# Performance work log

Hardware: AMD Instinct MI355X
Metric: run time of the kernel (lower is better)

## Reference

```python
import jax, jax.numpy as jnp
import numpy as np

H, DH = 16, 64  # heads, dim_head

def _ln(x, g, b):
    mu = jnp.mean(x, axis=-1, keepdims=True)
    var = jnp.var(x, axis=-1, keepdims=True)
    return (x - mu) * jax.lax.rsqrt(var + 1e-5) * g + b

def setup_inputs() -> dict:
    key = jax.random.key(0)
    ks = jax.random.split(key, 6)
    B, N1, N2, D = 8, 4096, 256, 1024
    inner = H * DH
    x = jax.random.normal(ks[0], (B, N1, D), jnp.float32)
    latents = jax.random.normal(ks[1], (B, N2, D), jnp.float32)
    mask = jnp.ones((B, N1 + N2), jnp.int32)
    Wq = jax.random.normal(ks[2], (D, inner), jnp.float32) / np.float32(np.sqrt(D))
    Wkv = jax.random.normal(ks[3], (D, 2 * inner), jnp.float32) / np.float32(np.sqrt(D))
    Wout = jax.random.normal(ks[4], (inner, D), jnp.float32) / np.float32(np.sqrt(inner))
    g_media = jnp.ones((D,), jnp.float32)
    b_media = jnp.zeros((D,), jnp.float32)
    g_lat = jnp.ones((D,), jnp.float32)
    b_lat = jnp.zeros((D,), jnp.float32)
    return {"x": x, "latents": latents, "mask": mask,
            "g_media": g_media, "b_media": b_media, "g_lat": g_lat, "b_lat": b_lat,
            "Wq": Wq, "Wkv": Wkv, "Wout": Wout}

def reference(x, latents, mask, g_media, b_media, g_lat, b_lat, Wq, Wkv, Wout):
    scale = DH ** -0.5
    xn = _ln(x, g_media, b_media)            # (B, N1, D)
    ln = _ln(latents, g_lat, b_lat)          # (B, N2, D)
    q = ln @ Wq                              # (B, N2, H*DH)
    kv = jnp.concatenate([xn, ln], axis=1) @ Wkv  # (B, N1+N2, 2*H*DH)
    k, v = jnp.split(kv, 2, axis=-1)
    B, N2 = q.shape[0], q.shape[1]
    Nk = k.shape[1]
    q = q.reshape(B, N2, H, DH).transpose(0, 2, 1, 3) * scale  # (B,H,N2,DH)
    k = k.reshape(B, Nk, H, DH).transpose(0, 2, 1, 3)
    v = v.reshape(B, Nk, H, DH).transpose(0, 2, 1, 3)
    sim = jnp.einsum('bhid,bhjd->bhij', q, k)                  # (B,H,N2,Nk)
    sim = sim - jax.lax.stop_gradient(jnp.max(sim, axis=-1, keepdims=True))
    sim = jnp.where(mask[:, None, None, :] == 0, jnp.float32(-10000.0), sim)
    attn = jax.nn.softmax(sim, axis=-1)
    out = jnp.einsum('bhij,bhjd->bhid', attn, v)               # (B,H,N2,DH)
    out = out.transpose(0, 2, 1, 3).reshape(B, N2, H * DH)
    return out @ Wout                                          # (B, N2, D)
```

## Files before the change

kernel.cpp:

```cpp
#include <hip/hip_runtime.h>
#include <stdint.h>

typedef __attribute__((ext_vector_type(4))) float f32x4;
typedef __attribute__((ext_vector_type(4))) int   i32x4;

__device__ __forceinline__ ushort f2bf(float f) {
  union { float f; uint32_t u; } v; v.f = f;
  uint32_t r = v.u + 0x7FFFu + ((v.u >> 16) & 1u);
  return (ushort)(r >> 16);
}
__device__ __forceinline__ float bf2f(ushort u) {
  union { uint32_t u; float f; } v; v.u = ((uint32_t)u) << 16; return v.f;
}
__device__ __forceinline__ void mfma_acc(f32x4& c, i32x4 a, i32x4 b) {
  asm volatile("v_mfma_f32_16x16x32_bf16 %0, %1, %2, %0" : "+v"(c) : "v"(a), "v"(b));
}
__device__ __forceinline__ void gload_lds16(const void* g, void* lds) {
  __builtin_amdgcn_global_load_lds(
      (const __attribute__((address_space(1))) void*)g,
      (__attribute__((address_space(3))) void*)lds, 16, 0, 0);
}

__global__ void __launch_bounds__(256) ln_kernel(
    const float* __restrict__ x, const float* __restrict__ lat,
    const float* __restrict__ gm, const float* __restrict__ bm,
    const float* __restrict__ gl, const float* __restrict__ bl,
    ushort* __restrict__ out) {
  int row = blockIdx.x;
  int b = row / 4352, j = row - b * 4352;
  const float *src, *g, *bi;
  if (j < 4096) { src = x + ((size_t)b * 4096 + j) * 1024; g = gm; bi = bm; }
  else          { src = lat + ((size_t)b * 256 + (j - 4096)) * 1024; g = gl; bi = bl; }
  int t = threadIdx.x;
  f32x4 v = ((const f32x4*)src)[t];
  float s = v.x + v.y + v.z + v.w;
  float q = v.x * v.x + v.y * v.y + v.z * v.z + v.w * v.w;
  #pragma unroll
  for (int o = 1; o < 64; o <<= 1) { s += __shfl_xor(s, o, 64); q += __shfl_xor(q, o, 64); }
  __shared__ float ss[4], sq[4];
  int w = t >> 6, l = t & 63;
  if (l == 0) { ss[w] = s; sq[w] = q; }
  __syncthreads();
  s = ss[0] + ss[1] + ss[2] + ss[3];
  q = sq[0] + sq[1] + sq[2] + sq[3];
  float mu = s * (1.f / 1024.f);
  float var = q * (1.f / 1024.f) - mu * mu;
  float rs = rsqrtf(var + 1e-5f);
  f32x4 gg = ((const f32x4*)g)[t], bb = ((const f32x4*)bi)[t];
  ushort4 o4;
  o4.x = f2bf((v.x - mu) * rs * gg.x + bb.x);
  o4.y = f2bf((v.y - mu) * rs * gg.y + bb.y);
  o4.z = f2bf((v.z - mu) * rs * gg.z + bb.z);
  o4.w = f2bf((v.w - mu) * rs * gg.w + bb.w);
  ((ushort4*)(out + (size_t)row * 1024))[t] = o4;
}

__global__ void __launch_bounds__(256) tsplit_kernel(
    const float* __restrict__ W, int K, int N, ushort* __restrict__ out, int K2, int write_lo) {
  int ntn = N >> 6;
  int tk = blockIdx.x / ntn, tn = blockIdx.x - tk * ntn;
  int k0 = tk * 32, n0 = tn * 64;
  __shared__ float tile[32][65];
  int t = threadIdx.x;
  #pragma unroll
  for (int i = 0; i < 8; i++) {
    int idx = t + i * 256;
    int k = idx >> 6, n = idx & 63;
    tile[k][n] = W[(size_t)(k0 + k) * N + n0 + n];
  }
  __syncthreads();
  #pragma unroll
  for (int i = 0; i < 8; i++) {
    int idx = t + i * 256;
    int n = idx >> 5, k = idx & 31;
    float v = tile[k][n];
    ushort hi = f2bf(v);
    size_t o = (size_t)(n0 + n) * K2 + k0 + k;
    out[o] = hi;
    if (write_lo) out[o + K] = f2bf(v - bf2f(hi));
  }
}

__global__ void __launch_bounds__(512, 2) gemm256_kv(
    const ushort* __restrict__ A, const ushort* __restrict__ Bw,
    ushort* __restrict__ okb, ushort* __restrict__ ovb) {
  int orig = blockIdx.x;
  int bx = (orig & 7) * 136 + (orig >> 3);
  int mt = bx >> 3, nt = bx & 7;
  int m0 = mt * 256, n0 = nt * 256;
  int t = threadIdx.x, w = t >> 6, l = t & 63, lg = l >> 4, lr = l & 15;
  int wr = w >> 2, wc = w & 3;

  __shared__ char smem[131072];

  auto stage = [&](int kt, int bsel) {
    size_t ka = (size_t)kt * 64;
    char* sA = smem + bsel * 65536;
    char* sB = smem + bsel * 65536 + 32768;
    #pragma unroll
    for (int i = 0; i < 4; i++) {
      int c = t + i * 512;
      int row = c >> 3, j = c & 7;
      int sj = j ^ (row & 7);
      gload_lds16(A + ((size_t)(m0 + row) * 1024 + ka + sj * 8), sA + c * 16);
    }
    #pragma unroll
    for (int i = 0; i < 4; i++) {
      int c = t + i * 512;
      int row = c >> 3, j = c & 7;
      int sj = j ^ (row & 7);
      gload_lds16(Bw + ((size_t)(n0 + row) * 1024 + ka + sj * 8), sB + c * 16);
    }
  };

  f32x4 acc[8][4];
  #pragma unroll
  for (int i = 0; i < 8; i++)
    #pragma unroll
    for (int j = 0; j < 4; j++) acc[i][j] = (f32x4){0.f, 0.f, 0.f, 0.f};

  stage(0, 0);
  stage(1, 1);
  const int swz = (lr & 7) << 4;

  for (int kt = 0; kt < 16; kt++) {
    if (kt < 15) asm volatile("s_waitcnt vmcnt(8)" ::: "memory");
    else         asm volatile("s_waitcnt vmcnt(0)" ::: "memory");
    __builtin_amdgcn_s_barrier();
    const char* cA = smem + (kt & 1) * 65536;
    const char* cB = smem + (kt & 1) * 65536 + 32768;
    i32x4 ar[4][2], br[4][2];
    #pragma unroll
    for (int mi = 0; mi < 4; mi++)
      #pragma unroll
      for (int kk = 0; kk < 2; kk++)
        ar[mi][kk] = *(const i32x4*)(cA + ((((wr * 128 + mi * 16 + lr) * 128) + kk * 64 + lg * 16) ^ swz));
    #pragma unroll
    for (int nj = 0; nj < 2; nj++)
      #pragma unroll
      for (int kk = 0; kk < 2; kk++)
        br[nj][kk] = *(const i32x4*)(cB + ((((wc * 64 + nj * 16 + lr) * 128) + kk * 64 + lg * 16) ^ swz));
    __builtin_amdgcn_s_setprio(1);
    #pragma unroll
    for (int mi = 0; mi < 4; mi++)
      #pragma unroll
      for (int nj = 0; nj < 2; nj++)
        #pragma unroll
        for (int kk = 0; kk < 2; kk++) mfma_acc(acc[mi][nj], ar[mi][kk], br[nj][kk]);
    __builtin_amdgcn_s_setprio(0);
    #pragma unroll
    for (int nj = 2; nj < 4; nj++)
      #pragma unroll
      for (int kk = 0; kk < 2; kk++)
        br[nj][kk] = *(const i32x4*)(cB + ((((wc * 64 + nj * 16 + lr) * 128) + kk * 64 + lg * 16) ^ swz));
    __builtin_amdgcn_s_setprio(1);
    #pragma unroll
    for (int mi = 0; mi < 4; mi++)
      #pragma unroll
      for (int nj = 2; nj < 4; nj++)
        #pragma unroll
        for (int kk = 0; kk < 2; kk++) mfma_acc(acc[mi][nj], ar[mi][kk], br[nj][kk]);
    __builtin_amdgcn_s_setprio(0);
    #pragma unroll
    for (int mi = 0; mi < 4; mi++)
      #pragma unroll
      for (int kk = 0; kk < 2; kk++)
        ar[mi][kk] = *(const i32x4*)(cA + ((((wr * 128 + (mi + 4) * 16 + lr) * 128) + kk * 64 + lg * 16) ^ swz));
    __builtin_amdgcn_s_setprio(1);
    #pragma unroll
    for (int mi = 0; mi < 4; mi++)
      #pragma unroll
      for (int nj = 2; nj < 4; nj++)
        #pragma unroll
        for (int kk = 0; kk < 2; kk++) mfma_acc(acc[mi + 4][nj], ar[mi][kk], br[nj][kk]);
    __builtin_amdgcn_s_setprio(0);
    __builtin_amdgcn_s_setprio(1);
    #pragma unroll
    for (int mi = 0; mi < 4; mi++)
      #pragma unroll
      for (int nj = 0; nj < 2; nj++)
        #pragma unroll
        for (int kk = 0; kk < 2; kk++) mfma_acc(acc[mi + 4][nj], ar[mi][kk], br[nj][kk]);
    __builtin_amdgcn_s_setprio(0);
    __builtin_amdgcn_s_barrier();
    if (kt + 2 < 16) stage(kt + 2, kt & 1);
  }

  #pragma unroll
  for (int mi = 0; mi < 8; mi++) {
    #pragma unroll
    for (int r = 0; r < 4; r++) {
      int row = m0 + wr * 128 + mi * 16 + lg * 4 + r;
      int b = row / 4352; int n = row - b * 4352;
      size_t base = (size_t)b * 4456448 + (size_t)n * 64;
      #pragma unroll
      for (int nj = 0; nj < 4; nj++) {
        int col = n0 + wc * 64 + nj * 16 + lr;
        int cc = col & 1023; int h = cc >> 6; int d = cc & 63;
        ushort* dst = (col < 1024) ? okb : ovb;
        dst[base + (size_t)h * 278528 + d] = f2bf(acc[mi][nj][r]);
      }
    }
  }
}

template<int MODE>
__global__ void __launch_bounds__(256, 2) gemm_nt(
    const ushort* __restrict__ A, const ushort* __restrict__ Bw,
    ushort* __restrict__ okb, float* __restrict__ of,
    int ntn, int Keff, int lda, int ldb) {
  int orig = blockIdx.x;
  int bx = ((orig & 7) * (gridDim.x >> 3)) + (orig >> 3);
  int m0 = (bx / ntn) * 128, n0 = (bx - (bx / ntn) * ntn) * 128;
  int t = threadIdx.x, w = t >> 6, l = t & 63, lg = l >> 4, lr = l & 15;
  int wr = w >> 1, wc = w & 1;
  __shared__ ushort As[128 * 32];
  __shared__ ushort Bs[128 * 32];
  f32x4 acc[4][4];
  #pragma unroll
  for (int i = 0; i < 4; i++)
    #pragma unroll
    for (int j = 0; j < 4; j++) acc[i][j] = (f32x4){0.f, 0.f, 0.f, 0.f};

  int nk = Keff >> 5;
  for (int kt = 0; kt < nk; kt++) {
    int ka = kt * 32;
    #pragma unroll
    for (int c2 = 0; c2 < 2; c2++) {
      int c = w * 2 + c2;
      int arow = m0 + c * 16 + (l >> 2);
      if (MODE == 1) arow = ((arow >> 8) * 4352) + 4096 + (arow & 255);
      gload_lds16(A + (size_t)arow * lda + ka + (l & 3) * 8, &As[c * 512]);
    }
    #pragma unroll
    for (int c2 = 0; c2 < 2; c2++) {
      int c = w * 2 + c2;
      int brow = n0 + c * 16 + (l >> 2);
      gload_lds16(Bw + (size_t)brow * ldb + ka + (l & 3) * 8, &Bs[c * 512]);
    }
    __syncthreads();
    i32x4 af[4], bf[4];
    #pragma unroll
    for (int mi = 0; mi < 4; mi++)
      af[mi] = *(const i32x4*)&As[(wr * 64 + mi * 16 + lr) * 32 + lg * 8];
    #pragma unroll
    for (int nj = 0; nj < 4; nj++)
      bf[nj] = *(const i32x4*)&Bs[(wc * 64 + nj * 16 + lr) * 32 + lg * 8];
    #pragma unroll
    for (int mi = 0; mi < 4; mi++)
      #pragma unroll
      for (int nj = 0; nj < 4; nj++) mfma_acc(acc[mi][nj], af[mi], bf[nj]);
    __syncthreads();
  }

  #pragma unroll
  for (int mi = 0; mi < 4; mi++) {
    #pragma unroll
    for (int r = 0; r < 4; r++) {
      int row = m0 + wr * 64 + mi * 16 + lg * 4 + r;
      if (MODE == 1) {
        int b = row >> 8; int n2 = row & 255;
        size_t base = (size_t)b * 262144 + (size_t)n2 * 64;
        #pragma unroll
        for (int nj = 0; nj < 4; nj++) {
          int col = n0 + wc * 64 + nj * 16 + lr;
          int h = col >> 6; int d = col & 63;
          okb[base + (size_t)h * 16384 + d] = f2bf(acc[mi][nj][r] * 0.125f);
        }
      } else {
        #pragma unroll
        for (int nj = 0; nj < 4; nj++) {
          int col = n0 + wc * 64 + nj * 16 + lr;
          of[(size_t)row * 1024 + col] = acc[mi][nj][r];
        }
      }
    }
  }
}

__global__ void __launch_bounds__(256) vtrans_kernel(const ushort* __restrict__ v,
                                                     ushort* __restrict__ vt) {
  int bh = blockIdx.x / 68, tk = blockIdx.x - bh * 68;
  __shared__ ushort tl[64][65];
  int t = threadIdx.x;
  const ushort* src = v + (size_t)bh * 278528 + (size_t)tk * 4096;
  #pragma unroll
  for (int c2 = 0; c2 < 2; c2++) {
    int idx = t + c2 * 256;
    int row = idx >> 3, cb = idx & 7;
    i32x4 d4 = *(const i32x4*)(src + row * 64 + cb * 8);
    const ushort* p = (const ushort*)&d4;
    #pragma unroll
    for (int e = 0; e < 8; e++) tl[row][cb * 8 + e] = p[e];
  }
  __syncthreads();
  ushort* dst = vt + (size_t)bh * 278528 + tk * 64;
  #pragma unroll
  for (int i = 0; i < 16; i++) {
    int idx = t + i * 256;
    int d = idx >> 6, key = idx & 63;
    dst[(size_t)d * 4352 + key] = tl[key][d];
  }
}

__global__ void __launch_bounds__(256, 2) attn_kernel(
    const ushort* __restrict__ qb, const ushort* __restrict__ kb,
    const ushort* __restrict__ vt, const int* __restrict__ mask,
    ushort* __restrict__ ao) {
  int orig = blockIdx.x;
  int bid = ((orig & 7) << 6) + (orig >> 3);
  int qt = bid & 3; int h = (bid >> 2) & 15; int b = bid >> 6;
  int t = threadIdx.x, w = t >> 6, l = t & 63, lg = l >> 4, lr = l & 15;
  __shared__ ushort Kl[2][4096];
  __shared__ ushort Vl[2][4096];
  __shared__ ushort Pl[64 * 72];
  __shared__ float bias[4352];
  size_t bh = (size_t)b * 16 + h;
  const ushort* qhead = qb + bh * 16384 + (size_t)qt * 4096;
  const ushort* khead = kb + bh * 278528;
  const ushort* vthead = vt + bh * 278528;

  #pragma unroll
  for (int c2 = 0; c2 < 2; c2++) {
    int c = w * 2 + c2;
    int row = c * 8 + (l >> 3);
    int colb = ((l & 7) * 16) ^ ((row & 7) << 4);
    gload_lds16((const char*)qhead + row * 128 + colb, (char*)Kl + c * 1024);
  }
  for (int i = t; i < 4352; i += 256)
    bias[i] = mask[b * 4352 + i] ? -24.0f : -10024.0f;
  __syncthreads();
  i32x4 aq[2];
  #pragma unroll
  for (int kh = 0; kh < 2; kh++) {
    int row = w * 16 + lr;
    int off = (row * 128 + kh * 64 + lg * 16) ^ ((row & 7) << 4);
    aq[kh] = *(const i32x4*)((const char*)Kl + off);
  }
  __syncthreads();

  auto stage = [&](int tk, int bsel) {
    #pragma unroll
    for (int c2 = 0; c2 < 2; c2++) {
      int c = w * 2 + c2;
      int row = c * 8 + (l >> 3);
      int colb = ((l & 7) * 16) ^ ((row & 7) << 4);
      gload_lds16((const char*)khead + (size_t)(tk * 64 + row) * 128 + colb,
                  (char*)Kl + bsel * 8192 + c * 1024);
      gload_lds16((const char*)vthead + (size_t)row * 8704 + (size_t)tk * 128 + colb,
                  (char*)Vl + bsel * 8192 + c * 1024);
    }
  };

  float lsum[4];
  f32x4 oacc[4];
  #pragma unroll
  for (int r = 0; r < 4; r++) lsum[r] = 0.f;
  #pragma unroll
  for (int df = 0; df < 4; df++) oacc[df] = (f32x4){0.f, 0.f, 0.f, 0.f};

  stage(0, 0);
  int cur = 0;
  for (int tk = 0; tk < 68; tk++) {
    if (tk < 67) {
      stage(tk + 1, cur ^ 1);
      asm volatile("s_waitcnt vmcnt(4)" ::: "memory");
    } else {
      asm volatile("s_waitcnt vmcnt(0)" ::: "memory");
    }
    asm volatile("s_barrier" ::: "memory");
    const char* Kb = (const char*)Kl + cur * 8192;
    const char* Vb = (const char*)Vl + cur * 8192;

    f32x4 sf[4];
    #pragma unroll
    for (int kf = 0; kf < 4; kf++) {
      f32x4 s = (f32x4){0.f, 0.f, 0.f, 0.f};
      #pragma unroll
      for (int kh = 0; kh < 2; kh++) {
        int row = kf * 16 + lr;
        int off = (row * 128 + kh * 64 + lg * 16) ^ ((row & 7) << 4);
        i32x4 bk = *(const i32x4*)(Kb + off);
        mfma_acc(s, aq[kh], bk);
      }
      sf[kf] = s;
    }
    #pragma unroll
    for (int kf = 0; kf < 4; kf++) {
      float ma = bias[tk * 64 + kf * 16 + lr];
      #pragma unroll
      for (int r = 0; r < 4; r++) {
        float p = __expf(sf[kf][r] + ma);
        lsum[r] += p;
        Pl[(w * 16 + lg * 4 + r) * 72 + kf * 16 + lr] = f2bf(p);
      }
    }
    #pragma unroll
    for (int kq = 0; kq < 2; kq++) {
      i32x4 ap = *(const i32x4*)&Pl[(w * 16 + lr) * 72 + kq * 32 + lg * 8];
      #pragma unroll
      for (int df = 0; df < 4; df++) {
        int row = df * 16 + lr;
        int off = (row * 128 + kq * 64 + lg * 16) ^ ((row & 7) << 4);
        i32x4 bv = *(const i32x4*)(Vb + off);
        mfma_acc(oacc[df], ap, bv);
      }
    }
    asm volatile("s_barrier" ::: "memory");
    cur ^= 1;
  }
  #pragma unroll
  for (int o = 1; o < 16; o <<= 1)
    #pragma unroll
    for (int r = 0; r < 4; r++) lsum[r] += __shfl_xor(lsum[r], o, 64);
  #pragma unroll
  for (int r = 0; r < 4; r++) lsum[r] = 1.f / lsum[r];
  int n2 = qt * 64 + w * 16 + lg * 4;
  #pragma unroll
  for (int df = 0; df < 4; df++)
    #pragma unroll
    for (int r = 0; r < 4; r++) {
      float vv = oacc[df][r] * lsum[r];
      ao[((size_t)b * 256 + (n2 + r)) * 1024 + h * 64 + df * 16 + lr] = f2bf(vv);
    }
}

extern "C" void kernel_launch(void* const* d_in, const int* in_sizes, int n_in,
                              void* d_out, int out_size, void* d_ws, size_t ws_size,
                              hipStream_t stream) {
  const float* x    = (const float*)d_in[0];
  const float* lat  = (const float*)d_in[1];
  const int*   msk  = (const int*)d_in[2];
  const float* gm   = (const float*)d_in[3];
  const float* bm   = (const float*)d_in[4];
  const float* gl   = (const float*)d_in[5];
  const float* bl   = (const float*)d_in[6];
  const float* Wq   = (const float*)d_in[7];
  const float* Wkv  = (const float*)d_in[8];
  const float* Wout = (const float*)d_in[9];
  float* out = (float*)d_out;
  char* ws = (char*)d_ws;

  ushort* xcat  = (ushort*)(ws);
  ushort* kbuf  = (ushort*)(ws + 71303168);
  ushort* vbuf  = (ushort*)(ws + 142606336);
  ushort* qbuf  = (ushort*)(ws + 213909504);
  ushort* aobuf = (ushort*)(ws + 218103808);
  ushort* wkvt  = (ushort*)(ws + 222298112);
  ushort* wqt   = (ushort*)(ws + 226492416);
  ushort* wot   = (ushort*)(ws + 228589568);
  ushort* vt    = xcat;

  ln_kernel<<<34816, 256, 0, stream>>>(x, lat, gm, bm, gl, bl, xcat);
  tsplit_kernel<<<32 * 32, 256, 0, stream>>>(Wkv, 1024, 2048, wkvt, 1024, 0);
  tsplit_kernel<<<32 * 16, 256, 0, stream>>>(Wq, 1024, 1024, wqt, 1024, 0);
  tsplit_kernel<<<32 * 16, 256, 0, stream>>>(Wout, 1024, 1024, wot, 1024, 0);
  gemm256_kv<<<1088, 512, 0, stream>>>(xcat, wkvt, kbuf, vbuf);
  gemm_nt<1><<<16 * 8, 256, 0, stream>>>(xcat, wqt, qbuf, nullptr, 8, 1024, 1024, 1024);
  vtrans_kernel<<<128 * 68, 256, 0, stream>>>(vbuf, vt);
  attn_kernel<<<512, 256, 0, stream>>>(qbuf, kbuf, vt, msk, aobuf);
  gemm_nt<2><<<16 * 8, 256, 0, stream>>>(aobuf, wot, nullptr, out, 8, 1024, 1024, 1024);
}
```

Before: 378.1 us.

## Fuse V transpose into KV GEMM epilogue via LDS staging

The KV GEMM epilogue now writes V directly in transposed (d-major) layout by staging each wave's accumulator tile in shared memory and emitting 16-byte vector stores, which removes the separate vtrans kernel and its extra global read/write of V. The inner MFMA loop is also reordered so all B fragments load up front and A rows 4-7 load into separate registers, changing register pressure and LDS read scheduling. Rows that cross a batch boundary fall back to scalar stores.

```diff
diff --git a/kernel.cpp b/kernel.cpp
--- a/kernel.cpp
+++ b/kernel.cpp
@@ -129,50 +129,42 @@
     __builtin_amdgcn_s_barrier();
     const char* cA = smem + (kt & 1) * 65536;
     const char* cB = smem + (kt & 1) * 65536 + 32768;
-    i32x4 ar[4][2], br[4][2];
+    i32x4 a03[4][2], a47[4][2], b01[2][2], b23[2][2];
     #pragma unroll
     for (int mi = 0; mi < 4; mi++)
       #pragma unroll
       for (int kk = 0; kk < 2; kk++)
-        ar[mi][kk] = *(const i32x4*)(cA + ((((wr * 128 + mi * 16 + lr) * 128) + kk * 64 + lg * 16) ^ swz));
+        a03[mi][kk] = *(const i32x4*)(cA + ((((wr * 128 + mi * 16 + lr) * 128) + kk * 64 + lg * 16) ^ swz));
     #pragma unroll
     for (int nj = 0; nj < 2; nj++)
       #pragma unroll
       for (int kk = 0; kk < 2; kk++)
-        br[nj][kk] = *(const i32x4*)(cB + ((((wc * 64 + nj * 16 + lr) * 128) + kk * 64 + lg * 16) ^ swz));
+        b01[nj][kk] = *(const i32x4*)(cB + ((((wc * 64 + nj * 16 + lr) * 128) + kk * 64 + lg * 16) ^ swz));
+    #pragma unroll
+    for (int nj = 0; nj < 2; nj++)
+      #pragma unroll
+      for (int kk = 0; kk < 2; kk++)
+        b23[nj][kk] = *(const i32x4*)(cB + ((((wc * 64 + (nj + 2) * 16 + lr) * 128) + kk * 64 + lg * 16) ^ swz));
     __builtin_amdgcn_s_setprio(1);
     #pragma unroll
     for (int mi = 0; mi < 4; mi++)
       #pragma unroll
       for (int nj = 0; nj < 2; nj++)
         #pragma unroll
-        for (int kk = 0; kk < 2; kk++) mfma_acc(acc[mi][nj], ar[mi][kk], br[nj][kk]);
+        for (int kk = 0; kk < 2; kk++) mfma_acc(acc[mi][nj], a03[mi][kk], b01[nj][kk]);
     __builtin_amdgcn_s_setprio(0);
     #pragma unroll
-    for (int nj = 2; nj < 4; nj++)
+    for (int mi = 0; mi < 4; mi++)
       #pragma unroll
       for (int kk = 0; kk < 2; kk++)
-        br[nj][kk] = *(const i32x4*)(cB + ((((wc * 64 + nj * 16 + lr) * 128) + kk * 64 + lg * 16) ^ swz));
+        a47[mi][kk] = *(const i32x4*)(cA + ((((wr * 128 + (mi + 4) * 16 + lr) * 128) + kk * 64 + lg * 16) ^ swz));
     __builtin_amdgcn_s_setprio(1);
     #pragma unroll
     for (int mi = 0; mi < 4; mi++)
       #pragma unroll
-      for (int nj = 2; nj < 4; nj++)
-        #pragma unroll
-        for (int kk = 0; kk < 2; kk++) mfma_acc(acc[mi][nj], ar[mi][kk], br[nj][kk]);
-    __builtin_amdgcn_s_setprio(0);
-    #pragma unroll
-    for (int mi = 0; mi < 4; mi++)
-      #pragma unroll
-      for (int kk = 0; kk < 2; kk++)
-        ar[mi][kk] = *(const i32x4*)(cA + ((((wr * 128 + (mi + 4) * 16 + lr) * 128) + kk * 64 + lg * 16) ^ swz));
-    __builtin_amdgcn_s_setprio(1);
-    #pragma unroll
-    for (int mi = 0; mi < 4; mi++)
-      #pragma unroll
-      for (int nj = 2; nj < 4; nj++)
-        #pragma unroll
-        for (int kk = 0; kk < 2; kk++) mfma_acc(acc[mi + 4][nj], ar[mi][kk], br[nj][kk]);
+      for (int nj = 0; nj < 2; nj++)
+        #pragma unroll
+        for (int kk = 0; kk < 2; kk++) mfma_acc(acc[mi][nj + 2], a03[mi][kk], b23[nj][kk]);
     __builtin_amdgcn_s_setprio(0);
     __builtin_amdgcn_s_setprio(1);
     #pragma unroll
@@ -180,25 +172,71 @@
       #pragma unroll
       for (int nj = 0; nj < 2; nj++)
         #pragma unroll
-        for (int kk = 0; kk < 2; kk++) mfma_acc(acc[mi + 4][nj], ar[mi][kk], br[nj][kk]);
+        for (int kk = 0; kk < 2; kk++) mfma_acc(acc[mi + 4][nj + 2], a47[mi][kk], b23[nj][kk]);
+    __builtin_amdgcn_s_setprio(0);
+    __builtin_amdgcn_s_setprio(1);
+    #pragma unroll
+    for (int mi = 0; mi < 4; mi++)
+      #pragma unroll
+      for (int nj = 0; nj < 2; nj++)
+        #pragma unroll
+        for (int kk = 0; kk < 2; kk++) mfma_acc(acc[mi + 4][nj], a47[mi][kk], b01[nj][kk]);
     __builtin_amdgcn_s_setprio(0);
     __builtin_amdgcn_s_barrier();
     if (kt + 2 < 16) stage(kt + 2, kt & 1);
   }
 
-  #pragma unroll
-  for (int mi = 0; mi < 8; mi++) {
-    #pragma unroll
-    for (int r = 0; r < 4; r++) {
-      int row = m0 + wr * 128 + mi * 16 + lg * 4 + r;
-      int b = row / 4352; int n = row - b * 4352;
-      size_t base = (size_t)b * 4456448 + (size_t)n * 64;
-      #pragma unroll
-      for (int nj = 0; nj < 4; nj++) {
-        int col = n0 + wc * 64 + nj * 16 + lr;
-        int cc = col & 1023; int h = cc >> 6; int d = cc & 63;
-        ushort* dst = (col < 1024) ? okb : ovb;
-        dst[base + (size_t)h * 278528 + d] = f2bf(acc[mi][nj][r]);
+  if (n0 < 1024) {
+    #pragma unroll
+    for (int mi = 0; mi < 8; mi++) {
+      #pragma unroll
+      for (int r = 0; r < 4; r++) {
+        int row = m0 + wr * 128 + mi * 16 + lg * 4 + r;
+        int b = row / 4352; int n = row - b * 4352;
+        size_t base = (size_t)b * 4456448 + (size_t)n * 64;
+        #pragma unroll
+        for (int nj = 0; nj < 4; nj++) {
+          int col = n0 + wc * 64 + nj * 16 + lr;
+          int h = col >> 6; int d = col & 63;
+          okb[base + (size_t)h * 278528 + d] = f2bf(acc[mi][nj][r]);
+        }
+      }
+    }
+  } else {
+    ushort* trp = (ushort*)(smem + w * 8704);
+    int hh = ((n0 - 1024) + wc * 64) >> 6;
+    size_t hoff = (size_t)hh * 278528;
+    #pragma unroll
+    for (int p = 0; p < 2; p++) {
+      #pragma unroll
+      for (int njd = 0; njd < 2; njd++)
+        #pragma unroll
+        for (int mi = 0; mi < 8; mi++)
+          #pragma unroll
+          for (int r = 0; r < 4; r++)
+            trp[(njd * 16 + lr) * 136 + mi * 16 + lg * 4 + r] = f2bf(acc[mi][p * 2 + njd][r]);
+      #pragma unroll
+      for (int it = 0; it < 8; it++) {
+        int c = it * 4 + (l >> 4);
+        int rr8 = (l & 15) * 8;
+        i32x4 vdat = *(const i32x4*)&trp[c * 136 + rr8];
+        int d = p * 32 + c;
+        int row_g = m0 + wr * 128 + rr8;
+        int b0 = row_g / 4352;
+        int b7 = (row_g + 7) / 4352;
+        if (b0 == b7) {
+          size_t n = row_g - b0 * 4352;
+          *(i32x4*)(ovb + (size_t)b0 * 4456448 + hoff + (size_t)d * 4352 + n) = vdat;
+        } else {
+          const ushort* pv = (const ushort*)&vdat;
+          #pragma unroll
+          for (int e = 0; e < 8; e++) {
+            int rg = row_g + e;
+            int bb = rg / 4352;
+            int n = rg - bb * 4352;
+            ovb[(size_t)bb * 4456448 + hoff + (size_t)d * 4352 + n] = pv[e];
+          }
+        }
       }
     }
   }
@@ -275,31 +313,6 @@
         }
       }
     }
-  }
-}
-
-__global__ void __launch_bounds__(256) vtrans_kernel(const ushort* __restrict__ v,
-                                                     ushort* __restrict__ vt) {
-  int bh = blockIdx.x / 68, tk = blockIdx.x - bh * 68;
-  __shared__ ushort tl[64][65];
-  int t = threadIdx.x;
-  const ushort* src = v + (size_t)bh * 278528 + (size_t)tk * 4096;
-  #pragma unroll
-  for (int c2 = 0; c2 < 2; c2++) {
-    int idx = t + c2 * 256;
-    int row = idx >> 3, cb = idx & 7;
-    i32x4 d4 = *(const i32x4*)(src + row * 64 + cb * 8);
-    const ushort* p = (const ushort*)&d4;
-    #pragma unroll
-    for (int e = 0; e < 8; e++) tl[row][cb * 8 + e] = p[e];
-  }
-  __syncthreads();
-  ushort* dst = vt + (size_t)bh * 278528 + tk * 64;
-  #pragma unroll
-  for (int i = 0; i < 16; i++) {
-    int idx = t + i * 256;
-    int d = idx >> 6, key = idx & 63;
-    dst[(size_t)d * 4352 + key] = tl[key][d];
   }
 }
 
@@ -443,21 +456,19 @@
 
   ushort* xcat  = (ushort*)(ws);
   ushort* kbuf  = (ushort*)(ws + 71303168);
-  ushort* vbuf  = (ushort*)(ws + 142606336);
+  ushort* vtb   = (ushort*)(ws + 142606336);
   ushort* qbuf  = (ushort*)(ws + 213909504);
   ushort* aobuf = (ushort*)(ws + 218103808);
   ushort* wkvt  = (ushort*)(ws + 222298112);
   ushort* wqt   = (ushort*)(ws + 226492416);
   ushort* wot   = (ushort*)(ws + 228589568);
-  ushort* vt    = xcat;
 
   ln_kernel<<<34816, 256, 0, stream>>>(x, lat, gm, bm, gl, bl, xcat);
   tsplit_kernel<<<32 * 32, 256, 0, stream>>>(Wkv, 1024, 2048, wkvt, 1024, 0);
   tsplit_kernel<<<32 * 16, 256, 0, stream>>>(Wq, 1024, 1024, wqt, 1024, 0);
   tsplit_kernel<<<32 * 16, 256, 0, stream>>>(Wout, 1024, 1024, wot, 1024, 0);
-  gemm256_kv<<<1088, 512, 0, stream>>>(xcat, wkvt, kbuf, vbuf);
+  gemm256_kv<<<1088, 512, 0, stream>>>(xcat, wkvt, kbuf, vtb);
   gemm_nt<1><<<16 * 8, 256, 0, stream>>>(xcat, wqt, qbuf, nullptr, 8, 1024, 1024, 1024);
-  vtrans_kernel<<<128 * 68, 256, 0, stream>>>(vbuf, vt);
-  attn_kernel<<<512, 256, 0, stream>>>(qbuf, kbuf, vt, msk, aobuf);
+  attn_kernel<<<512, 256, 0, stream>>>(qbuf, kbuf, vtb, msk, aobuf);
   gemm_nt<2><<<16 * 8, 256, 0, stream>>>(aobuf, wot, nullptr, out, 8, 1024, 1024, 1024);
 }
```

Measured after the change: 431.7 us. 1.14x slower.
